# Kernel optimization log

Hardware: AMD Instinct MI355X
Metric: run time of the kernel (lower is better)

## Reference

```python
import jax, jax.numpy as jnp
import numpy as np

D = 64
H = 4
HD = D // H
N_MOL, E_MOL = 2048, 32768
N_PROT, E_PROT = 8192, 262144
LN_EPS = 1e-5


def _lin_params(key, d_in, d_out):
    k1, k2 = jax.random.split(key)
    lim = 1.0 / np.sqrt(d_in)
    w = jax.random.uniform(k1, (d_in, d_out), minval=-lim, maxval=lim, dtype=jnp.float32)
    b = jax.random.uniform(k2, (d_out,), minval=-lim, maxval=lim, dtype=jnp.float32)
    return w, b


def setup_inputs() -> dict:
    key = jax.random.key(0)
    ks = jax.random.split(key, 20)
    inp = {
        'x_mol': jax.random.normal(ks[0], (N_MOL, D), dtype=jnp.float32),
        'edge_index_mol': jax.random.randint(ks[1], (2, E_MOL), 0, N_MOL),
        'edge_attr_mol': jax.random.normal(ks[2], (E_MOL, D), dtype=jnp.float32),
        'x_prot': jax.random.normal(ks[3], (N_PROT, D), dtype=jnp.float32),
        'edge_index_prot': jax.random.randint(ks[4], (2, E_PROT), 0, N_PROT),
        'edge_attr_prot': jax.random.normal(ks[5], (E_PROT, D), dtype=jnp.float32),
    }
    # GINE MLPs: Linear -> ReLU -> Linear
    inp['mol_w1'], inp['mol_b1'] = _lin_params(ks[6], D, D)
    inp['mol_w2'], inp['mol_b2'] = _lin_params(ks[7], D, D)
    inp['prot_w1'], inp['prot_b1'] = _lin_params(ks[8], D, D)
    inp['prot_w2'], inp['prot_b2'] = _lin_params(ks[9], D, D)
    # cross-attn mol->prot (query=mol, key/value=prot)
    inp['mp_wq'], inp['mp_bq'] = _lin_params(ks[10], D, D)
    inp['mp_wk'], inp['mp_bk'] = _lin_params(ks[11], D, D)
    inp['mp_wv'], inp['mp_bv'] = _lin_params(ks[12], D, D)
    # cross-attn prot->mol (query=prot, key/value=mol)
    inp['pm_wq'], inp['pm_bq'] = _lin_params(ks[13], D, D)
    inp['pm_wk'], inp['pm_bk'] = _lin_params(ks[14], D, D)
    inp['pm_wv'], inp['pm_bv'] = _lin_params(ks[15], D, D)
    # layer norms
    inp['ln_mol_g'] = jnp.ones((D,), jnp.float32)
    inp['ln_mol_b'] = jnp.zeros((D,), jnp.float32)
    inp['ln_prot_g'] = jnp.ones((D,), jnp.float32)
    inp['ln_prot_b'] = jnp.zeros((D,), jnp.float32)
    return inp


def _gine_conv(x, edge_index, edge_attr, w1, b1, w2, b2, n_nodes):
    # message: relu(x_j + edge_attr); aggregate: mean at target; update: MLP((1+eps)*x + aggr), eps=0
    src, dst = edge_index[0], edge_index[1]
    msg = jax.nn.relu(x[src] + edge_attr)                       # [E, D]
    ssum = jax.ops.segment_sum(msg, dst, num_segments=n_nodes)  # [N, D]
    cnt = jax.ops.segment_sum(jnp.ones((msg.shape[0],), msg.dtype), dst, num_segments=n_nodes)
    aggr = ssum / jnp.maximum(cnt, 1.0)[:, None]
    h = x + aggr
    h = jax.nn.relu(h @ w1 + b1) @ w2 + b2
    return h


def _cross_attn(q_nodes, k_nodes, wq, bq, wk, bk, wv, bv):
    Nq, Nk = q_nodes.shape[0], k_nodes.shape[0]
    Q = (q_nodes @ wq + bq).reshape(Nq, H, HD)
    K = (k_nodes @ wk + bk).reshape(Nk, H, HD)
    V = (k_nodes @ wv + bv).reshape(Nk, H, HD)
    scores = jnp.einsum('qhd,khd->hqk', Q, K) / np.sqrt(HD).astype(np.float32)
    attn = jax.nn.softmax(scores, axis=-1)                      # [H, Nq, Nk]
    out = jnp.einsum('hqk,khd->qhd', attn, V).reshape(Nq, D)
    return out


def _layer_norm(x, g, b):
    mu = jnp.mean(x, axis=-1, keepdims=True)
    var = jnp.mean(jnp.square(x - mu), axis=-1, keepdims=True)
    return (x - mu) * jax.lax.rsqrt(var + LN_EPS) * g + b


def reference(x_mol, edge_index_mol, edge_attr_mol, x_prot, edge_index_prot, edge_attr_prot,
              mol_w1, mol_b1, mol_w2, mol_b2, prot_w1, prot_b1, prot_w2, prot_b2,
              mp_wq, mp_bq, mp_wk, mp_bk, mp_wv, mp_bv,
              pm_wq, pm_bq, pm_wk, pm_bk, pm_wv, pm_bv,
              ln_mol_g, ln_mol_b, ln_prot_g, ln_prot_b):
    h_mol = jax.nn.relu(_gine_conv(x_mol, edge_index_mol, edge_attr_mol,
                                   mol_w1, mol_b1, mol_w2, mol_b2, x_mol.shape[0]))
    h_prot = jax.nn.relu(_gine_conv(x_prot, edge_index_prot, edge_attr_prot,
                                    prot_w1, prot_b1, prot_w2, prot_b2, x_prot.shape[0]))
    h_mol_attn = _cross_attn(h_mol, h_prot, mp_wq, mp_bq, mp_wk, mp_bk, mp_wv, mp_bv)
    h_prot_attn = _cross_attn(h_prot, h_mol, pm_wq, pm_bq, pm_wk, pm_bk, pm_wv, pm_bv)
    out_mol = _layer_norm(h_mol + h_mol_attn, ln_mol_g, ln_mol_b)
    out_prot = _layer_norm(h_prot + h_prot_attn, ln_prot_g, ln_prot_b)
    return out_mol, out_prot
```

## Files before the change

kernel.cpp:

```cpp
#include <hip/hip_runtime.h>

#define NM 2048
#define EM 32768
#define NP 8192
#define EP 262144

typedef __attribute__((ext_vector_type(8))) short short8;
typedef __attribute__((ext_vector_type(4))) float f32x4;
typedef __attribute__((ext_vector_type(16))) float f32x16;

#define LOG2E 1.44269504088896340736f

__device__ __forceinline__ float e2(float x) { return __builtin_amdgcn_exp2f(x); }
__device__ __forceinline__ unsigned int pk_bf16_tr(float a, float b) {
    return __builtin_amdgcn_perm(__float_as_uint(a), __float_as_uint(b), 0x03020706u);
}
__device__ __forceinline__ unsigned short cvt_bf16(float f) {
    unsigned int u = __float_as_uint(f);
    u = (u + 0x7fff + ((u >> 16) & 1)) >> 16;
    return (unsigned short)u;
}

__global__ __launch_bounds__(256) void hist_kernel(
    const int* __restrict__ ei_m, const int* __restrict__ ei_p,
    int* __restrict__ cnt_m, int* __restrict__ cnt_p)
{
    int idx = blockIdx.x * 256 + threadIdx.x;
    if (idx < EM) atomicAdd(&cnt_m[ei_m[EM + idx]], 1);
    int j = idx - EM;
    if (j >= 0 && j < EP) atomicAdd(&cnt_p[ei_p[EP + j]], 1);
}

__global__ __launch_bounds__(256) void scan_kernel(
    const int* __restrict__ cnt_m, const int* __restrict__ cnt_p,
    int* __restrict__ start_m, int* __restrict__ start_p,
    int* __restrict__ cur_m, int* __restrict__ cur_p)
{
    const int* cnt; int* start; int* cur; int n;
    if (blockIdx.x == 0) { cnt = cnt_m; start = start_m; cur = cur_m; n = NM; }
    else                 { cnt = cnt_p; start = start_p; cur = cur_p; n = NP; }
    int per = n >> 8;
    int tid = threadIdx.x;
    int base = tid * per;
    int s = 0;
    for (int i = 0; i < per; i++) s += cnt[base + i];
    __shared__ int wsum[4];
    int lane = tid & 63, w = tid >> 6;
    int v = s;
    #pragma unroll
    for (int off = 1; off < 64; off <<= 1) {
        int u = __shfl_up(v, off, 64);
        if (lane >= off) v += u;
    }
    if (lane == 63) wsum[w] = v;
    __syncthreads();
    int wo = 0;
    for (int i = 0; i < w; i++) wo += wsum[i];
    int run = wo + v - s;
    for (int i = 0; i < per; i++) {
        start[base + i] = run; cur[base + i] = run;
        run += cnt[base + i];
    }
    if (tid == 255) start[n] = run;
}

__global__ __launch_bounds__(256) void scatter_kernel(
    const int* __restrict__ ei_m, const int* __restrict__ ei_p,
    int* __restrict__ cur_m, int* __restrict__ cur_p,
    int* __restrict__ pidx_m, int* __restrict__ pidx_p)
{
    int idx = blockIdx.x * 256 + threadIdx.x;
    if (idx < EM) {
        int d = ei_m[EM + idx];
        int pos = atomicAdd(&cur_m[d], 1);
        pidx_m[pos] = (idx << 11) | ei_m[idx];
    }
    int j = idx - EM;
    if (j >= 0 && j < EP) {
        int d = ei_p[EP + j];
        int pos = atomicAdd(&cur_p[d], 1);
        pidx_p[pos] = (j << 13) | ei_p[j];
    }
}

__global__ __launch_bounds__(256) void node_aggr_kernel(
    const float* __restrict__ x_m, const float* __restrict__ ea_m,
    const int* __restrict__ start_m, const int* __restrict__ pidx_m,
    const float* __restrict__ x_p, const float* __restrict__ ea_p,
    const int* __restrict__ start_p, const int* __restrict__ pidx_p,
    float* __restrict__ h0_m, float* __restrict__ h0_p)
{
    int wave = threadIdx.x >> 6, lane = threadIdx.x & 63;
    int nid = blockIdx.x * 4 + wave;
    const float *x, *ea; const int *start, *pidx; float* h0; int n, sh, msk;
    if (nid < NM) { x = x_m; ea = ea_m; start = start_m; pidx = pidx_m; h0 = h0_m; n = nid; sh = 11; msk = 2047; }
    else          { x = x_p; ea = ea_p; start = start_p; pidx = pidx_p; h0 = h0_p; n = nid - NM; sh = 13; msk = 8191; }
    int b  = __builtin_amdgcn_readfirstlane(start[n]);
    int e  = __builtin_amdgcn_readfirstlane(start[n + 1]);
    int deg = e - b;
    const int* pp = pidx + b;
    float acc = 0.f;
    int j = 0;
    for (; j + 8 <= deg; j += 8) {
        int v0 = __builtin_amdgcn_readfirstlane(pp[j]);
        int v1 = __builtin_amdgcn_readfirstlane(pp[j + 1]);
        int v2 = __builtin_amdgcn_readfirstlane(pp[j + 2]);
        int v3 = __builtin_amdgcn_readfirstlane(pp[j + 3]);
        int v4 = __builtin_amdgcn_readfirstlane(pp[j + 4]);
        int v5 = __builtin_amdgcn_readfirstlane(pp[j + 5]);
        int v6 = __builtin_amdgcn_readfirstlane(pp[j + 6]);
        int v7 = __builtin_amdgcn_readfirstlane(pp[j + 7]);
        float a0 = ea[(size_t)(((unsigned)v0) >> sh) * 64 + lane];
        float a1 = ea[(size_t)(((unsigned)v1) >> sh) * 64 + lane];
        float a2 = ea[(size_t)(((unsigned)v2) >> sh) * 64 + lane];
        float a3 = ea[(size_t)(((unsigned)v3) >> sh) * 64 + lane];
        float a4 = ea[(size_t)(((unsigned)v4) >> sh) * 64 + lane];
        float a5 = ea[(size_t)(((unsigned)v5) >> sh) * 64 + lane];
        float a6 = ea[(size_t)(((unsigned)v6) >> sh) * 64 + lane];
        float a7 = ea[(size_t)(((unsigned)v7) >> sh) * 64 + lane];
        float y0 = x[(size_t)(v0 & msk) * 64 + lane];
        float y1 = x[(size_t)(v1 & msk) * 64 + lane];
        float y2 = x[(size_t)(v2 & msk) * 64 + lane];
        float y3 = x[(size_t)(v3 & msk) * 64 + lane];
        float y4 = x[(size_t)(v4 & msk) * 64 + lane];
        float y5 = x[(size_t)(v5 & msk) * 64 + lane];
        float y6 = x[(size_t)(v6 & msk) * 64 + lane];
        float y7 = x[(size_t)(v7 & msk) * 64 + lane];
        acc += fmaxf(y0 + a0, 0.f); acc += fmaxf(y1 + a1, 0.f);
        acc += fmaxf(y2 + a2, 0.f); acc += fmaxf(y3 + a3, 0.f);
        acc += fmaxf(y4 + a4, 0.f); acc += fmaxf(y5 + a5, 0.f);
        acc += fmaxf(y6 + a6, 0.f); acc += fmaxf(y7 + a7, 0.f);
    }
    for (; j < deg; ++j) {
        int v0 = __builtin_amdgcn_readfirstlane(pp[j]);
        acc += fmaxf(x[(size_t)(v0 & msk) * 64 + lane] + ea[(size_t)(((unsigned)v0) >> sh) * 64 + lane], 0.f);
    }
    float aggr = acc / fmaxf((float)deg, 1.f);
    h0[(size_t)n * 64 + lane] = x[(size_t)n * 64 + lane] + aggr;
}

__global__ __launch_bounds__(256) void mlp_qkv_kernel(
    const float* __restrict__ h0_m, const float* __restrict__ h0_p,
    const float* __restrict__ w1m, const float* __restrict__ b1m,
    const float* __restrict__ w2m, const float* __restrict__ b2m,
    const float* __restrict__ w1p, const float* __restrict__ b1p,
    const float* __restrict__ w2p, const float* __restrict__ b2p,
    const float* __restrict__ wq_m, const float* __restrict__ bq_m,
    const float* __restrict__ wk_m, const float* __restrict__ bk_m,
    const float* __restrict__ wv_m, const float* __restrict__ bv_m,
    const float* __restrict__ wq_p, const float* __restrict__ bq_p,
    const float* __restrict__ wk_p, const float* __restrict__ bk_p,
    const float* __restrict__ wv_p, const float* __restrict__ bv_p,
    float* __restrict__ hm, float* __restrict__ hp,
    unsigned short* __restrict__ Qm, unsigned short* __restrict__ Km, unsigned short* __restrict__ Vtm,
    unsigned short* __restrict__ Qp, unsigned short* __restrict__ Kp, unsigned short* __restrict__ Vtp,
    int* __restrict__ norms)
{
    const float *h0, *w1, *b1, *w2, *b2, *wq, *bq, *wk, *bk, *wv, *bv;
    float* hout; unsigned short *Q, *K, *Vt; int row0, N, nbase;
    if (blockIdx.x < NM / 32) {
        h0 = h0_m; w1 = w1m; b1 = b1m; w2 = w2m; b2 = b2m;
        wq = wq_m; bq = bq_m; wk = wk_m; bk = bk_m; wv = wv_m; bv = bv_m;
        hout = hm; Q = Qm; K = Km; Vt = Vtm; N = NM; row0 = blockIdx.x * 32; nbase = 0;
    } else {
        h0 = h0_p; w1 = w1p; b1 = b1p; w2 = w2p; b2 = b2p;
        wq = wq_p; bq = bq_p; wk = wk_p; bk = bk_p; wv = wv_p; bv = bv_p;
        hout = hp; Q = Qp; K = Kp; Vt = Vtp; N = NP; row0 = (blockIdx.x - NM / 32) * 32; nbase = 2;
    }
    __shared__ float sWa[4096], sWb[4096], sWc[4096];
    __shared__ float sb1[64], sb2[64], sbq[64], sbk[64], sbv[64];
    __shared__ float sh0[32][64], sh1[32][64];
    __shared__ float rmx[8];
    int t = threadIdx.x;
    for (int i = t; i < 4096; i += 256) { sWa[i] = w1[i]; sWb[i] = w2[i]; sWc[i] = wq[i]; }
    if (t < 64) { sb1[t] = b1[t]; sb2[t] = b2[t]; sbq[t] = bq[t]; sbk[t] = bk[t]; sbv[t] = bv[t]; }
    for (int i = t; i < 32 * 64; i += 256) {
        int r = i >> 6, c = i & 63;
        sh0[r][c] = h0[(size_t)(row0 + r) * 64 + c];
    }
    __syncthreads();
    int j = t & 63, rs = t >> 6;
    for (int r = rs; r < 32; r += 4) {
        float a = sb1[j];
        #pragma unroll
        for (int c = 0; c < 64; c++) a += sh0[r][c] * sWa[c * 64 + j];
        sh1[r][j] = fmaxf(a, 0.0f);
    }
    __syncthreads();
    for (int r = rs; r < 32; r += 4) {
        float a = sb2[j];
        #pragma unroll
        for (int c = 0; c < 64; c++) a += sh1[r][c] * sWb[c * 64 + j];
        float hval = fmaxf(a, 0.0f);
        hout[(size_t)(row0 + r) * 64 + j] = hval;
        sh0[r][j] = hval;
    }
    for (int i = t; i < 4096; i += 256) sWa[i] = wk[i];
    __syncthreads();
    float qmx = 0.f, kmx = 0.f;
    for (int r = rs; r < 32; r += 4) {
        float aq = sbq[j], ak = sbk[j];
        #pragma unroll
        for (int c = 0; c < 64; c++) {
            float h = sh0[r][c];
            aq += h * sWc[c * 64 + j];
            ak += h * sWa[c * 64 + j];
        }
        float qs = aq * (0.25f * LOG2E);
        size_t o = (size_t)(row0 + r) * 64 + j;
        Q[o] = cvt_bf16(qs);
        K[o] = cvt_bf16(ak);
        float qsq = qs * qs, ksq = ak * ak;
        #pragma unroll
        for (int o2 = 1; o2 <= 8; o2 <<= 1) {
            qsq += __shfl_xor(qsq, o2, 64);
            ksq += __shfl_xor(ksq, o2, 64);
        }
        qmx = fmaxf(qmx, qsq);
        kmx = fmaxf(kmx, ksq);
    }
    for (int i = t; i < 4096; i += 256) sWb[i] = wv[i];
    qmx = fmaxf(qmx, __shfl_xor(qmx, 16, 64)); qmx = fmaxf(qmx, __shfl_xor(qmx, 32, 64));
    kmx = fmaxf(kmx, __shfl_xor(kmx, 16, 64)); kmx = fmaxf(kmx, __shfl_xor(kmx, 32, 64));
    if (j == 0) { rmx[rs] = qmx; rmx[4 + rs] = kmx; }
    __syncthreads();
    for (int r = rs; r < 32; r += 4) {
        float av = sbv[j];
        #pragma unroll
        for (int c = 0; c < 64; c++) av += sh0[r][c] * sWb[c * 64 + j];
        Vt[(size_t)j * N + row0 + r] = cvt_bf16(av);
    }
    if (t == 0) {
        float q4 = fmaxf(fmaxf(rmx[0], rmx[1]), fmaxf(rmx[2], rmx[3]));
        float k4 = fmaxf(fmaxf(rmx[4], rmx[5]), fmaxf(rmx[6], rmx[7]));
        atomicMax(&norms[nbase],     __float_as_int(sqrtf(q4)));
        atomicMax(&norms[nbase + 1], __float_as_int(sqrtf(k4)));
    }
}

__global__ __launch_bounds__(256) void attn_kernel(
    const unsigned short* __restrict__ Qm, const unsigned short* __restrict__ Km,
    const unsigned short* __restrict__ Vtm,
    const unsigned short* __restrict__ Qp, const unsigned short* __restrict__ Kp,
    const unsigned short* __restrict__ Vtp,
    const int* __restrict__ norms, float* __restrict__ partial)
{
    __shared__ unsigned int plds[4][2][2][16][20];
    int t = threadIdx.x;
    int wave = t >> 6;
    int lane = t & 63;
    int qrow = lane & 15;
    int quad = lane >> 4;
    int q5   = lane & 31;
    int half = lane >> 5;
    int qtl  = q5 >> 4;
    int dwb  = half * 2;
    int W = blockIdx.x * 4 + wave;

    const unsigned short *Q, *K, *Vt; int Nk; float m;
    int chunk, h, qt2, Tbase, T1off;
    if (W < 2048) {
        Q = Qm; K = Kp; Vt = Vtp; Nk = NP;
        m = __int_as_float(norms[0]) * __int_as_float(norms[3]);
        chunk = W & 7; h = (W >> 3) & 3; qt2 = W >> 5;
        Tbase = W + qt2 * 32; T1off = 32;
    } else {
        int W2 = W - 2048;
        Q = Qp; K = Km; Vt = Vtm; Nk = NM;
        m = __int_as_float(norms[2]) * __int_as_float(norms[1]);
        chunk = W2 & 1; h = (W2 >> 1) & 3; qt2 = W2 >> 3;
        Tbase = 4096 + W2 + qt2 * 8; T1off = 8;
    }

    short8 qf = *(const short8*)(Q + ((size_t)(qt2 * 32 + q5)) * 64 + h * 16 + half * 8);

    const f32x16 zero16 = {0.f,0.f,0.f,0.f,0.f,0.f,0.f,0.f,0.f,0.f,0.f,0.f,0.f,0.f,0.f,0.f};
    const f32x4 zero4 = {0.f, 0.f, 0.f, 0.f};
    int kbase = chunk * 1024;
    const unsigned short* krow = K + (size_t)(kbase + q5) * 64 + h * 16 + half * 8;
    const unsigned short* vrow = Vt + ((size_t)(h * 16 + qrow)) * Nk + kbase + quad * 8;

    float l = 0.0f;
    f32x4 accA = zero4, accB = zero4;

    short8 kf_0, kf_1, vf_0, vf_1;
    kf_0 = *(const short8*)(krow);
    kf_1 = *(const short8*)(krow + 32 * 64);
    vf_0 = *(const short8*)(vrow);
    vf_1 = *(const short8*)(vrow + 32);

    short8 vf_prev;

#define QK_PHASE(IT, SLOT, BUF)                                                             \
    {                                                                                       \
        short8 kf = kf_##SLOT; short8 vf = vf_##SLOT;                                       \
        if ((IT) < 30) {                                                                    \
            int off = ((IT) + 2) * 32;                                                      \
            kf_##SLOT = *(const short8*)(krow + (size_t)off * 64);                          \
            vf_##SLOT = *(const short8*)(vrow + off);                                       \
        }                                                                                   \
        f32x16 s = __builtin_amdgcn_mfma_f32_32x32x16_bf16(kf, qf, zero16, 0, 0, 0);        \
        float p0  = e2(s[0] - m),  p1  = e2(s[1] - m),  p2  = e2(s[2] - m),  p3  = e2(s[3] - m);  \
        float p4  = e2(s[4] - m),  p5  = e2(s[5] - m),  p6  = e2(s[6] - m),  p7  = e2(s[7] - m);  \
        float p8  = e2(s[8] - m),  p9  = e2(s[9] - m),  p10 = e2(s[10] - m), p11 = e2(s[11] - m); \
        float p12 = e2(s[12] - m), p13 = e2(s[13] - m), p14 = e2(s[14] - m), p15 = e2(s[15] - m); \
        l += (((p0 + p1) + (p2 + p3)) + ((p4 + p5) + (p6 + p7)))                            \
           + (((p8 + p9) + (p10 + p11)) + ((p12 + p13) + (p14 + p15)));                     \
        uint2 w0; w0.x = pk_bf16_tr(p0, p1);   w0.y = pk_bf16_tr(p2, p3);                   \
        uint2 w1; w1.x = pk_bf16_tr(p4, p5);   w1.y = pk_bf16_tr(p6, p7);                   \
        uint2 w2; w2.x = pk_bf16_tr(p8, p9);   w2.y = pk_bf16_tr(p10, p11);                 \
        uint2 w3; w3.x = pk_bf16_tr(p12, p13); w3.y = pk_bf16_tr(p14, p15);                 \
        *(uint2*)&plds[wave][qtl][BUF][qrow][dwb]      = w0;                                \
        *(uint2*)&plds[wave][qtl][BUF][qrow][dwb + 4]  = w1;                                \
        *(uint2*)&plds[wave][qtl][BUF][qrow][dwb + 8]  = w2;                                \
        *(uint2*)&plds[wave][qtl][BUF][qrow][dwb + 12] = w3;                                \
        vf_cur = vf;                                                                        \
    }

#define STEP(IT, SLOT, BUF, PREV)                                                           \
    {                                                                                       \
        short8 pfA = *(short8*)&plds[wave][0][PREV][qrow][quad * 4];                        \
        short8 pfB = *(short8*)&plds[wave][1][PREV][qrow][quad * 4];                        \
        short8 vf_cur;                                                                      \
        QK_PHASE(IT, SLOT, BUF)                                                             \
        accA = __builtin_amdgcn_mfma_f32_16x16x32_bf16(vf_prev, pfA, accA, 0, 0, 0);        \
        accB = __builtin_amdgcn_mfma_f32_16x16x32_bf16(vf_prev, pfB, accB, 0, 0, 0);        \
        vf_prev = vf_cur;                                                                   \
    }

    {
        short8 vf_cur;
        QK_PHASE(0, 0, 0)
        vf_prev = vf_cur;
    }
    for (int p = 0; p < 15; ++p) {
        STEP(2 * p + 1, 1, 1, 0)
        STEP(2 * p + 2, 0, 0, 1)
    }
    STEP(31, 1, 1, 0)
    {
        short8 pfA = *(short8*)&plds[wave][0][1][qrow][quad * 4];
        short8 pfB = *(short8*)&plds[wave][1][1][qrow][quad * 4];
        accA = __builtin_amdgcn_mfma_f32_16x16x32_bf16(vf_prev, pfA, accA, 0, 0, 0);
        accB = __builtin_amdgcn_mfma_f32_16x16x32_bf16(vf_prev, pfB, accB, 0, 0, 0);
    }
#undef STEP
#undef QK_PHASE

    float ltot = l + __shfl_xor(l, 32, 64);

    float* pb0 = partial + (size_t)Tbase * 288;
    *(f32x4*)&pb0[qrow * 16 + quad * 4] = accA;
    float* pb1 = partial + (size_t)(Tbase + T1off) * 288;
    *(f32x4*)&pb1[qrow * 16 + quad * 4] = accB;
    if (lane < 16)       pb0[272 + q5] = ltot;
    else if (lane < 32)  pb1[272 + (q5 - 16)] = ltot;
}

__global__ __launch_bounds__(256) void merge_ln_kernel(
    const float* __restrict__ partial,
    const float* __restrict__ h_m, const float* __restrict__ h_p,
    const float* __restrict__ gm, const float* __restrict__ bm,
    const float* __restrict__ gp, const float* __restrict__ bp_,
    float* __restrict__ out)
{
    int t = threadIdx.x;
    int grow = blockIdx.x * 4 + (t >> 6);
    int c = t & 63;
    const float *pbase, *hbuf, *g, *bb; float* o; int NC, row;
    if (grow < NM) { pbase = partial;               hbuf = h_m; g = gm; bb = bm;  o = out;             NC = 8; row = grow; }
    else           { pbase = partial + 4096 * 288;  hbuf = h_p; g = gp; bb = bp_; o = out + NM * 64;   NC = 2; row = grow - NM; }
    int hi = c >> 4, d = c & 15;
    int qt = row >> 4, ql = row & 15;
    const float* base = pbase + (size_t)(qt * 4 + hi) * NC * 288;
    float L = 0.0f, A = 0.0f;
    for (int cc = 0; cc < NC; ++cc) {
        L += base[cc * 288 + 272 + ql];
        A += base[cc * 288 + ql * 16 + d];
    }
    float v = hbuf[(size_t)row * 64 + c] + A / L;
    float s = v;
    #pragma unroll
    for (int o2 = 32; o2 >= 1; o2 >>= 1) s += __shfl_xor(s, o2, 64);
    float mu = s * (1.0f / 64.0f);
    float dv = v - mu;
    float sq = dv * dv;
    #pragma unroll
    for (int o2 = 32; o2 >= 1; o2 >>= 1) sq += __shfl_xor(sq, o2, 64);
    float var = sq * (1.0f / 64.0f);
    o[(size_t)row * 64 + c] = dv * rsqrtf(var + 1e-5f) * g[c] + bb[c];
}

extern "C" void kernel_launch(void* const* d_in, const int* in_sizes, int n_in,
                              void* d_out, int out_size, void* d_ws, size_t ws_size,
                              hipStream_t stream)
{
    const float* x_mol   = (const float*)d_in[0];
    const int*   ei_mol  = (const int*)  d_in[1];
    const float* ea_mol  = (const float*)d_in[2];
    const float* x_prot  = (const float*)d_in[3];
    const int*   ei_prot = (const int*)  d_in[4];
    const float* ea_prot = (const float*)d_in[5];
    const float* mol_w1  = (const float*)d_in[6];
    const float* mol_b1  = (const float*)d_in[7];
    const float* mol_w2  = (const float*)d_in[8];
    const float* mol_b2  = (const float*)d_in[9];
    const float* prot_w1 = (const float*)d_in[10];
    const float* prot_b1 = (const float*)d_in[11];
    const float* prot_w2 = (const float*)d_in[12];
    const float* prot_b2 = (const float*)d_in[13];
    const float* mp_wq = (const float*)d_in[14]; const float* mp_bq = (const float*)d_in[15];
    const float* mp_wk = (const float*)d_in[16]; const float* mp_bk = (const float*)d_in[17];
    const float* mp_wv = (const float*)d_in[18]; const float* mp_bv = (const float*)d_in[19];
    const float* pm_wq = (const float*)d_in[20]; const float* pm_bq = (const float*)d_in[21];
    const float* pm_wk = (const float*)d_in[22]; const float* pm_bk = (const float*)d_in[23];
    const float* pm_wv = (const float*)d_in[24]; const float* pm_bv = (const float*)d_in[25];
    const float* ln_mol_g  = (const float*)d_in[26];
    const float* ln_mol_b  = (const float*)d_in[27];
    const float* ln_prot_g = (const float*)d_in[28];
    const float* ln_prot_b = (const float*)d_in[29];

    float* ws = (float*)d_ws;
    float* h_mol   = ws;
    float* h_prot  = h_mol + 131072;
    float* partial = h_prot + 524288;
    float* h0_mol  = partial;
    float* h0_prot = h0_mol + 131072;
    int* ip      = (int*)(partial + 2359296);
    int* cnt_m   = ip;
    int* cnt_p   = cnt_m + 2048;
    int* norms   = cnt_p + 8192;
    int* start_m = norms + 4;
    int* start_p = start_m + 2052;
    int* cur_m   = start_p + 8196;
    int* cur_p   = cur_m + 2048;
    int* pidx_m  = cur_p + 8192;
    int* pidx_p  = pidx_m + 32768;
    unsigned short* bf = (unsigned short*)(pidx_p + 262144);
    unsigned short* Qm  = bf;
    unsigned short* Km  = Qm + 131072;
    unsigned short* Vtm = Km + 131072;
    unsigned short* Qp  = Vtm + 131072;
    unsigned short* Kp  = Qp + 524288;
    unsigned short* Vtp = Kp + 524288;

    hipMemsetAsync(cnt_m, 0, (size_t)(2048 + 8192 + 4) * sizeof(int), stream);

    const int EB = (EM + EP) / 256;
    hist_kernel<<<EB, 256, 0, stream>>>(ei_mol, ei_prot, cnt_m, cnt_p);
    scan_kernel<<<2, 256, 0, stream>>>(cnt_m, cnt_p, start_m, start_p, cur_m, cur_p);
    scatter_kernel<<<EB, 256, 0, stream>>>(ei_mol, ei_prot, cur_m, cur_p, pidx_m, pidx_p);
    node_aggr_kernel<<<(NM + NP) / 4, 256, 0, stream>>>(
        x_mol, ea_mol, start_m, pidx_m,
        x_prot, ea_prot, start_p, pidx_p, h0_mol, h0_prot);

    mlp_qkv_kernel<<<(NM + NP) / 32, 256, 0, stream>>>(
        h0_mol, h0_prot,
        mol_w1, mol_b1, mol_w2, mol_b2, prot_w1, prot_b1, prot_w2, prot_b2,
        mp_wq, mp_bq, pm_wk, pm_bk, pm_wv, pm_bv,
        pm_wq, pm_bq, mp_wk, mp_bk, mp_wv, mp_bv,
        h_mol, h_prot, Qm, Km, Vtm, Qp, Kp, Vtp, norms);

    attn_kernel<<<1024, 256, 0, stream>>>(Qm, Km, Vtm, Qp, Kp, Vtp, norms, partial);

    float* out = (float*)d_out;
    merge_ln_kernel<<<(NM + NP) / 4, 256, 0, stream>>>(
        partial, h_mol, h_prot, ln_mol_g, ln_mol_b, ln_prot_g, ln_prot_b, out);
}
```

Before: 294.1 us.

## Run MLP and QKV projections on bf16 MFMA with pre-transposed weights

The MLP and Q/K/V projection kernel moves from scalar fp32 FMA loops over LDS-staged weights to bf16 16x16x32 MFMA instructions. A new prep kernel converts and transposes all ten weight matrices to bf16 once per call. node_aggr now writes h0 as bf16 so it can feed the MFMAs directly, and each wave handles 16 rows with a small per-wave LDS tile between layers, which removes block-wide syncs. This adds a kernel launch and bf16 rounding of the hidden activations and MLP weights, which costs some accuracy.

```diff
diff --git a/kernel.cpp b/kernel.cpp
--- a/kernel.cpp
+++ b/kernel.cpp
@@ -6,6 +6,7 @@
 #define EP 262144
 
 typedef __attribute__((ext_vector_type(8))) short short8;
+typedef __attribute__((ext_vector_type(4))) short short4v;
 typedef __attribute__((ext_vector_type(4))) float f32x4;
 typedef __attribute__((ext_vector_type(16))) float f32x16;
 
@@ -88,13 +89,13 @@
     const int* __restrict__ start_m, const int* __restrict__ pidx_m,
     const float* __restrict__ x_p, const float* __restrict__ ea_p,
     const int* __restrict__ start_p, const int* __restrict__ pidx_p,
-    float* __restrict__ h0_m, float* __restrict__ h0_p)
+    unsigned short* __restrict__ h0b_m, unsigned short* __restrict__ h0b_p)
 {
     int wave = threadIdx.x >> 6, lane = threadIdx.x & 63;
     int nid = blockIdx.x * 4 + wave;
-    const float *x, *ea; const int *start, *pidx; float* h0; int n, sh, msk;
-    if (nid < NM) { x = x_m; ea = ea_m; start = start_m; pidx = pidx_m; h0 = h0_m; n = nid; sh = 11; msk = 2047; }
-    else          { x = x_p; ea = ea_p; start = start_p; pidx = pidx_p; h0 = h0_p; n = nid - NM; sh = 13; msk = 8191; }
+    const float *x, *ea; const int *start, *pidx; unsigned short* h0b; int n, sh, msk;
+    if (nid < NM) { x = x_m; ea = ea_m; start = start_m; pidx = pidx_m; h0b = h0b_m; n = nid; sh = 11; msk = 2047; }
+    else          { x = x_p; ea = ea_p; start = start_p; pidx = pidx_p; h0b = h0b_p; n = nid - NM; sh = 13; msk = 8191; }
     int b  = __builtin_amdgcn_readfirstlane(start[n]);
     int e  = __builtin_amdgcn_readfirstlane(start[n + 1]);
     int deg = e - b;
@@ -136,105 +137,162 @@
         acc += fmaxf(x[(size_t)(v0 & msk) * 64 + lane] + ea[(size_t)(((unsigned)v0) >> sh) * 64 + lane], 0.f);
     }
     float aggr = acc / fmaxf((float)deg, 1.f);
-    h0[(size_t)n * 64 + lane] = x[(size_t)n * 64 + lane] + aggr;
+    h0b[(size_t)n * 64 + lane] = cvt_bf16(x[(size_t)n * 64 + lane] + aggr);
+}
+
+__global__ __launch_bounds__(256) void prep_w_kernel(
+    const float* __restrict__ w0, const float* __restrict__ w1, const float* __restrict__ w2,
+    const float* __restrict__ w3, const float* __restrict__ w4, const float* __restrict__ w5,
+    const float* __restrict__ w6, const float* __restrict__ w7, const float* __restrict__ w8,
+    const float* __restrict__ w9, unsigned short* __restrict__ wt)
+{
+    int b = blockIdx.x;
+    int t = b >> 4;
+    int e = (b & 15) * 256 + threadIdx.x;
+    const float* src;
+    switch (t) {
+        case 0: src = w0; break; case 1: src = w1; break; case 2: src = w2; break;
+        case 3: src = w3; break; case 4: src = w4; break; case 5: src = w5; break;
+        case 6: src = w6; break; case 7: src = w7; break; case 8: src = w8; break;
+        default: src = w9; break;
+    }
+    int n = e >> 6, k = e & 63;
+    wt[t * 4096 + e] = cvt_bf16(src[k * 64 + n]);
 }
 
 __global__ __launch_bounds__(256) void mlp_qkv_kernel(
-    const float* __restrict__ h0_m, const float* __restrict__ h0_p,
-    const float* __restrict__ w1m, const float* __restrict__ b1m,
-    const float* __restrict__ w2m, const float* __restrict__ b2m,
-    const float* __restrict__ w1p, const float* __restrict__ b1p,
-    const float* __restrict__ w2p, const float* __restrict__ b2p,
-    const float* __restrict__ wq_m, const float* __restrict__ bq_m,
-    const float* __restrict__ wk_m, const float* __restrict__ bk_m,
-    const float* __restrict__ wv_m, const float* __restrict__ bv_m,
-    const float* __restrict__ wq_p, const float* __restrict__ bq_p,
-    const float* __restrict__ wk_p, const float* __restrict__ bk_p,
-    const float* __restrict__ wv_p, const float* __restrict__ bv_p,
+    const unsigned short* __restrict__ h0b_m, const unsigned short* __restrict__ h0b_p,
+    const unsigned short* __restrict__ wt,
+    const float* __restrict__ b1m_, const float* __restrict__ b2m_,
+    const float* __restrict__ bqm_, const float* __restrict__ bkm_, const float* __restrict__ bvm_,
+    const float* __restrict__ b1p_, const float* __restrict__ b2p_,
+    const float* __restrict__ bqp_, const float* __restrict__ bkp_, const float* __restrict__ bvp_,
     float* __restrict__ hm, float* __restrict__ hp,
     unsigned short* __restrict__ Qm, unsigned short* __restrict__ Km, unsigned short* __restrict__ Vtm,
     unsigned short* __restrict__ Qp, unsigned short* __restrict__ Kp, unsigned short* __restrict__ Vtp,
     int* __restrict__ norms)
 {
-    const float *h0, *w1, *b1, *w2, *b2, *wq, *bq, *wk, *bk, *wv, *bv;
-    float* hout; unsigned short *Q, *K, *Vt; int row0, N, nbase;
-    if (blockIdx.x < NM / 32) {
-        h0 = h0_m; w1 = w1m; b1 = b1m; w2 = w2m; b2 = b2m;
-        wq = wq_m; bq = bq_m; wk = wk_m; bk = bk_m; wv = wv_m; bv = bv_m;
-        hout = hm; Q = Qm; K = Km; Vt = Vtm; N = NM; row0 = blockIdx.x * 32; nbase = 0;
+    __shared__ unsigned short tile[4][2][16][72];
+    int t = threadIdx.x, wave = t >> 6, lane = t & 63;
+    int col = lane & 15, quad = lane >> 4;
+    int blk = blockIdx.x;
+    const unsigned short* h0b; const float *b1, *b2, *bq, *bk, *bv;
+    float* hout; unsigned short *Q, *K, *Vt; int N, row0, wofs, nb;
+    if (blk < NM / 64) {
+        h0b = h0b_m; b1 = b1m_; b2 = b2m_; bq = bqm_; bk = bkm_; bv = bvm_;
+        hout = hm; Q = Qm; K = Km; Vt = Vtm; N = NM;
+        row0 = blk * 64 + wave * 16; wofs = 0; nb = 0;
     } else {
-        h0 = h0_p; w1 = w1p; b1 = b1p; w2 = w2p; b2 = b2p;
-        wq = wq_p; bq = bq_p; wk = wk_p; bk = bk_p; wv = wv_p; bv = bv_p;
-        hout = hp; Q = Qp; K = Kp; Vt = Vtp; N = NP; row0 = (blockIdx.x - NM / 32) * 32; nbase = 2;
-    }
-    __shared__ float sWa[4096], sWb[4096], sWc[4096];
-    __shared__ float sb1[64], sb2[64], sbq[64], sbk[64], sbv[64];
-    __shared__ float sh0[32][64], sh1[32][64];
-    __shared__ float rmx[8];
-    int t = threadIdx.x;
-    for (int i = t; i < 4096; i += 256) { sWa[i] = w1[i]; sWb[i] = w2[i]; sWc[i] = wq[i]; }
-    if (t < 64) { sb1[t] = b1[t]; sb2[t] = b2[t]; sbq[t] = bq[t]; sbk[t] = bk[t]; sbv[t] = bv[t]; }
-    for (int i = t; i < 32 * 64; i += 256) {
-        int r = i >> 6, c = i & 63;
-        sh0[r][c] = h0[(size_t)(row0 + r) * 64 + c];
-    }
-    __syncthreads();
-    int j = t & 63, rs = t >> 6;
-    for (int r = rs; r < 32; r += 4) {
-        float a = sb1[j];
+        h0b = h0b_p; b1 = b1p_; b2 = b2p_; bq = bqp_; bk = bkp_; bv = bvp_;
+        hout = hp; Q = Qp; K = Kp; Vt = Vtp; N = NP;
+        row0 = (blk - NM / 64) * 64 + wave * 16; wofs = 5 * 4096; nb = 2;
+    }
+    const f32x4 zero4 = {0.f, 0.f, 0.f, 0.f};
+    const unsigned short* wb = wt + wofs + (size_t)col * 64 + quad * 8;
+
+    const unsigned short* ar = h0b + (size_t)(row0 + col) * 64 + quad * 8;
+    short8 aL = *(const short8*)ar;
+    short8 aH = *(const short8*)(ar + 32);
+
+    #pragma unroll
+    for (int nt = 0; nt < 4; ++nt) {
+        short8 bL = *(const short8*)(wb + nt * 1024);
+        short8 bH = *(const short8*)(wb + nt * 1024 + 32);
+        f32x4 d = __builtin_amdgcn_mfma_f32_16x16x32_bf16(aL, bL, zero4, 0, 0, 0);
+        d = __builtin_amdgcn_mfma_f32_16x16x32_bf16(aH, bH, d, 0, 0, 0);
+        float bias = b1[nt * 16 + col];
         #pragma unroll
-        for (int c = 0; c < 64; c++) a += sh0[r][c] * sWa[c * 64 + j];
-        sh1[r][j] = fmaxf(a, 0.0f);
-    }
-    __syncthreads();
-    for (int r = rs; r < 32; r += 4) {
-        float a = sb2[j];
+        for (int r = 0; r < 4; ++r)
+            tile[wave][0][quad * 4 + r][nt * 16 + col] = cvt_bf16(fmaxf(d[r] + bias, 0.f));
+    }
+    short8 a1L = *(const short8*)&tile[wave][0][col][quad * 8];
+    short8 a1H = *(const short8*)&tile[wave][0][col][32 + quad * 8];
+
+    #pragma unroll
+    for (int nt = 0; nt < 4; ++nt) {
+        short8 bL = *(const short8*)(wb + 4096 + nt * 1024);
+        short8 bH = *(const short8*)(wb + 4096 + nt * 1024 + 32);
+        f32x4 d = __builtin_amdgcn_mfma_f32_16x16x32_bf16(a1L, bL, zero4, 0, 0, 0);
+        d = __builtin_amdgcn_mfma_f32_16x16x32_bf16(a1H, bH, d, 0, 0, 0);
+        float bias = b2[nt * 16 + col];
         #pragma unroll
-        for (int c = 0; c < 64; c++) a += sh1[r][c] * sWb[c * 64 + j];
-        float hval = fmaxf(a, 0.0f);
-        hout[(size_t)(row0 + r) * 64 + j] = hval;
-        sh0[r][j] = hval;
-    }
-    for (int i = t; i < 4096; i += 256) sWa[i] = wk[i];
-    __syncthreads();
-    float qmx = 0.f, kmx = 0.f;
-    for (int r = rs; r < 32; r += 4) {
-        float aq = sbq[j], ak = sbk[j];
+        for (int r = 0; r < 4; ++r) {
+            float v = fmaxf(d[r] + bias, 0.f);
+            hout[(size_t)(row0 + quad * 4 + r) * 64 + nt * 16 + col] = v;
+            tile[wave][1][quad * 4 + r][nt * 16 + col] = cvt_bf16(v);
+        }
+    }
+    short8 a2L = *(const short8*)&tile[wave][1][col][quad * 8];
+    short8 a2H = *(const short8*)&tile[wave][1][col][32 + quad * 8];
+
+    float q2[4] = {0.f, 0.f, 0.f, 0.f};
+    #pragma unroll
+    for (int nt = 0; nt < 4; ++nt) {
+        short8 bL = *(const short8*)(wb + 2 * 4096 + nt * 1024);
+        short8 bH = *(const short8*)(wb + 2 * 4096 + nt * 1024 + 32);
+        f32x4 d = __builtin_amdgcn_mfma_f32_16x16x32_bf16(a2L, bL, zero4, 0, 0, 0);
+        d = __builtin_amdgcn_mfma_f32_16x16x32_bf16(a2H, bH, d, 0, 0, 0);
+        float bias = bq[nt * 16 + col];
         #pragma unroll
-        for (int c = 0; c < 64; c++) {
-            float h = sh0[r][c];
-            aq += h * sWc[c * 64 + j];
-            ak += h * sWa[c * 64 + j];
+        for (int r = 0; r < 4; ++r) {
+            float qv = (d[r] + bias) * (0.25f * LOG2E);
+            Q[(size_t)(row0 + quad * 4 + r) * 64 + nt * 16 + col] = cvt_bf16(qv);
+            q2[r] += qv * qv;
         }
-        float qs = aq * (0.25f * LOG2E);
-        size_t o = (size_t)(row0 + r) * 64 + j;
-        Q[o] = cvt_bf16(qs);
-        K[o] = cvt_bf16(ak);
-        float qsq = qs * qs, ksq = ak * ak;
+    }
+    float qmx = 0.f;
+    #pragma unroll
+    for (int r = 0; r < 4; ++r) {
+        float s = q2[r];
+        s += __shfl_xor(s, 1, 64); s += __shfl_xor(s, 2, 64);
+        s += __shfl_xor(s, 4, 64); s += __shfl_xor(s, 8, 64);
+        qmx = fmaxf(qmx, s);
+    }
+
+    float k2[4] = {0.f, 0.f, 0.f, 0.f};
+    #pragma unroll
+    for (int nt = 0; nt < 4; ++nt) {
+        short8 bL = *(const short8*)(wb + 3 * 4096 + nt * 1024);
+        short8 bH = *(const short8*)(wb + 3 * 4096 + nt * 1024 + 32);
+        f32x4 d = __builtin_amdgcn_mfma_f32_16x16x32_bf16(a2L, bL, zero4, 0, 0, 0);
+        d = __builtin_amdgcn_mfma_f32_16x16x32_bf16(a2H, bH, d, 0, 0, 0);
+        float bias = bk[nt * 16 + col];
         #pragma unroll
-        for (int o2 = 1; o2 <= 8; o2 <<= 1) {
-            qsq += __shfl_xor(qsq, o2, 64);
-            ksq += __shfl_xor(ksq, o2, 64);
+        for (int r = 0; r < 4; ++r) {
+            float kv = d[r] + bias;
+            K[(size_t)(row0 + quad * 4 + r) * 64 + nt * 16 + col] = cvt_bf16(kv);
+            k2[r] += kv * kv;
         }
-        qmx = fmaxf(qmx, qsq);
-        kmx = fmaxf(kmx, ksq);
-    }
-    for (int i = t; i < 4096; i += 256) sWb[i] = wv[i];
+    }
+    float kmx = 0.f;
+    #pragma unroll
+    for (int r = 0; r < 4; ++r) {
+        float s = k2[r];
+        s += __shfl_xor(s, 1, 64); s += __shfl_xor(s, 2, 64);
+        s += __shfl_xor(s, 4, 64); s += __shfl_xor(s, 8, 64);
+        kmx = fmaxf(kmx, s);
+    }
+
+    #pragma unroll
+    for (int nt = 0; nt < 4; ++nt) {
+        short8 bL = *(const short8*)(wb + 4 * 4096 + nt * 1024);
+        short8 bH = *(const short8*)(wb + 4 * 4096 + nt * 1024 + 32);
+        f32x4 d = __builtin_amdgcn_mfma_f32_16x16x32_bf16(a2L, bL, zero4, 0, 0, 0);
+        d = __builtin_amdgcn_mfma_f32_16x16x32_bf16(a2H, bH, d, 0, 0, 0);
+        float bias = bv[nt * 16 + col];
+        short4v vv;
+        vv.x = (short)cvt_bf16(d[0] + bias);
+        vv.y = (short)cvt_bf16(d[1] + bias);
+        vv.z = (short)cvt_bf16(d[2] + bias);
+        vv.w = (short)cvt_bf16(d[3] + bias);
+        *(short4v*)(Vt + (size_t)(nt * 16 + col) * N + row0 + quad * 4) = vv;
+    }
+
     qmx = fmaxf(qmx, __shfl_xor(qmx, 16, 64)); qmx = fmaxf(qmx, __shfl_xor(qmx, 32, 64));
     kmx = fmaxf(kmx, __shfl_xor(kmx, 16, 64)); kmx = fmaxf(kmx, __shfl_xor(kmx, 32, 64));
-    if (j == 0) { rmx[rs] = qmx; rmx[4 + rs] = kmx; }
-    __syncthreads();
-    for (int r = rs; r < 32; r += 4) {
-        float av = sbv[j];
-        #pragma unroll
-        for (int c = 0; c < 64; c++) av += sh0[r][c] * sWb[c * 64 + j];
-        Vt[(size_t)j * N + row0 + r] = cvt_bf16(av);
-    }
-    if (t == 0) {
-        float q4 = fmaxf(fmaxf(rmx[0], rmx[1]), fmaxf(rmx[2], rmx[3]));
-        float k4 = fmaxf(fmaxf(rmx[4], rmx[5]), fmaxf(rmx[6], rmx[7]));
-        atomicMax(&norms[nbase],     __float_as_int(sqrtf(q4)));
-        atomicMax(&norms[nbase + 1], __float_as_int(sqrtf(k4)));
+    if (lane == 0) {
+        atomicMax(&norms[nb],     __float_as_int(sqrtf(qmx)));
+        atomicMax(&norms[nb + 1], __float_as_int(sqrtf(kmx)));
     }
 }
 
@@ -424,8 +482,8 @@
     float* h_mol   = ws;
     float* h_prot  = h_mol + 131072;
     float* partial = h_prot + 524288;
-    float* h0_mol  = partial;
-    float* h0_prot = h0_mol + 131072;
+    unsigned short* h0b_mol  = (unsigned short*)partial;
+    unsigned short* h0b_prot = h0b_mol + 131072;
     int* ip      = (int*)(partial + 2359296);
     int* cnt_m   = ip;
     int* cnt_p   = cnt_m + 2048;
@@ -443,8 +501,13 @@
     unsigned short* Qp  = Vtm + 131072;
     unsigned short* Kp  = Qp + 524288;
     unsigned short* Vtp = Kp + 524288;
+    unsigned short* wt  = Vtp + 524288;
 
     hipMemsetAsync(cnt_m, 0, (size_t)(2048 + 8192 + 4) * sizeof(int), stream);
+
+    prep_w_kernel<<<160, 256, 0, stream>>>(
+        mol_w1, mol_w2, mp_wq, pm_wk, pm_wv,
+        prot_w1, prot_w2, pm_wq, mp_wk, mp_wv, wt);
 
     const int EB = (EM + EP) / 256;
     hist_kernel<<<EB, 256, 0, stream>>>(ei_mol, ei_prot, cnt_m, cnt_p);
@@ -452,13 +515,12 @@
     scatter_kernel<<<EB, 256, 0, stream>>>(ei_mol, ei_prot, cur_m, cur_p, pidx_m, pidx_p);
     node_aggr_kernel<<<(NM + NP) / 4, 256, 0, stream>>>(
         x_mol, ea_mol, start_m, pidx_m,
-        x_prot, ea_prot, start_p, pidx_p, h0_mol, h0_prot);
-
-    mlp_qkv_kernel<<<(NM + NP) / 32, 256, 0, stream>>>(
-        h0_mol, h0_prot,
-        mol_w1, mol_b1, mol_w2, mol_b2, prot_w1, prot_b1, prot_w2, prot_b2,
-        mp_wq, mp_bq, pm_wk, pm_bk, pm_wv, pm_bv,
-        pm_wq, pm_bq, mp_wk, mp_bk, mp_wv, mp_bv,
+        x_prot, ea_prot, start_p, pidx_p, h0b_mol, h0b_prot);
+
+    mlp_qkv_kernel<<<(NM + NP) / 64, 256, 0, stream>>>(
+        h0b_mol, h0b_prot, wt,
+        mol_b1, mol_b2, mp_bq, pm_bk, pm_bv,
+        prot_b1, prot_b2, pm_bq, mp_bk, mp_bv,
         h_mol, h_prot, Qm, Km, Vtm, Qp, Kp, Vtp, norms);
 
     attn_kernel<<<1024, 256, 0, stream>>>(Qm, Km, Vtm, Qp, Kp, Vtp, norms, partial);
```

Result: no change. 290.3 us (-1.3%).
